# Optimization experiments

Hardware: AMD Instinct MI355X
Metric: run time of the kernel (lower is better)

## Reference

```python
import jax, jax.numpy as jnp
import numpy as np

N_EMBD = 256  # scale uses input channel dim C, per original code


def setup_inputs() -> dict:
    key = jax.random.key(0)
    k1, k2, k3, k4 = jax.random.split(key, 4)
    B, T, C, H = 512, 256, 256, 64
    x = jax.random.normal(k1, (B, T, C), dtype=jnp.float32)
    Wq = jax.random.normal(k2, (C, H), dtype=jnp.float32) * (C ** -0.5)
    Wk = jax.random.normal(k3, (C, H), dtype=jnp.float32) * (C ** -0.5)
    Wv = jax.random.normal(k4, (C, H), dtype=jnp.float32) * (C ** -0.5)
    return {"x": x, "Wq": Wq, "Wk": Wk, "Wv": Wv}


def reference(x, Wq, Wk, Wv):
    B, T, C = x.shape
    q = jnp.einsum("btc,ch->bth", x, Wq)  # [B,T,H]
    k = jnp.einsum("btc,ch->bth", x, Wk)
    v = jnp.einsum("btc,ch->bth", x, Wv)
    # Note: original scales by C**-0.5 (input dim), not head_size**-0.5.
    scores = jnp.einsum("bqh,bkh->bqk", q, k) * (C ** -0.5)  # [B,T,T]
    causal = jnp.tril(jnp.ones((T, T), dtype=bool))
    scores = jnp.where(causal, scores, -jnp.inf)
    weights = jax.nn.softmax(scores, axis=-1)
    # Dropout is identity at inference (Keras default training=False).
    out = jnp.einsum("bqk,bkh->bqh", weights, v)  # [B,T,H]
    return out
```

## Files before the change

kernel.cpp:

```cpp
#include <hip/hip_runtime.h>

#define B_  512
#define T_  256
#define C_  256
#define H_  64
#define BT_ (B_ * T_)

typedef unsigned short u16;
typedef __attribute__((ext_vector_type(8))) __bf16 bf16x8;
typedef __attribute__((ext_vector_type(8))) u16 u16x8;
typedef __attribute__((ext_vector_type(4))) float f32x4;

__device__ __forceinline__ u16 f2bf(float f) {
  union { float f; unsigned u; } v; v.f = f;
  unsigned r = v.u + 0x7fffu + ((v.u >> 16) & 1u);
  return (u16)(r >> 16);
}

__device__ __forceinline__ f32x4 mfma16(bf16x8 a, bf16x8 b, f32x4 c) {
  return __builtin_amdgcn_mfma_f32_16x16x32_bf16(a, b, c, 0, 0, 0);
}

__global__ __launch_bounds__(256) void wconv_kernel(
    const float* __restrict__ Wq, const float* __restrict__ Wk,
    const float* __restrict__ Wv, u16* __restrict__ wt) {
  int idx = blockIdx.x * 256 + threadIdx.x;
  int w   = idx >> 14;
  int rem = idx & 16383;
  int h   = rem >> 8;
  int c   = rem & 255;
  const float* W = (w == 0) ? Wq : (w == 1) ? Wk : Wv;
  wt[idx] = f2bf(W[c * H_ + h]);
}

__global__ __launch_bounds__(512, 2) void fused_kernel(
    const float* __restrict__ x, const u16* __restrict__ wt,
    float* __restrict__ out) {
  __shared__ u16 sB[2][192 * 40];
  __shared__ u16 sQ[256 * 72];
  __shared__ u16 sK[256 * 72];
  __shared__ u16 sVt[64 * 264];
  __shared__ u16 sP[8 * 16 * 88];

  const int tid  = threadIdx.x;
  const int wave = tid >> 6, lane = tid & 63;
  const int lr = lane & 15, lg = lane >> 4;
  const int b = blockIdx.x;

  const float* xb = x + (size_t)b * T_ * C_;
  float* ob = out + (size_t)b * T_ * H_;

  const f32x4 fzero = {0.f, 0.f, 0.f, 0.f};

  f32x4 acc[2][12];
#pragma unroll
  for (int mt = 0; mt < 2; ++mt)
#pragma unroll
    for (int nt = 0; nt < 12; ++nt) acc[mt][nt] = fzero;

  const float* xp0 = xb + (size_t)(wave * 32 + lr) * C_ + lg * 8;
  const float* xp1 = xp0 + 16 * C_;

  float4 aA[2][2][2];
  u16x8  breg[2][2];

#define LOAD_A(buf, kk)                                     \
  {                                                         \
    aA[buf][0][0] = *(const float4*)(xp0 + (kk) * 32);      \
    aA[buf][0][1] = *(const float4*)(xp0 + (kk) * 32 + 4);  \
    aA[buf][1][0] = *(const float4*)(xp1 + (kk) * 32);      \
    aA[buf][1][1] = *(const float4*)(xp1 + (kk) * 32 + 4);  \
  }

#define LOAD_B(buf, kk)                                                         \
  {                                                                             \
    int d0 = tid;                                                               \
    breg[buf][0] = *(const u16x8*)(wt + (d0 >> 2) * C_ + (kk) * 32 + (d0 & 3) * 8); \
    if (tid < 256) {                                                            \
      int d1 = 512 + tid;                                                       \
      breg[buf][1] = *(const u16x8*)(wt + (d1 >> 2) * C_ + (kk) * 32 + (d1 & 3) * 8); \
    }                                                                           \
  }

#define WRITE_B(buf)                                                \
  {                                                                 \
    int d0 = tid;                                                   \
    *(u16x8*)&sB[buf][(d0 >> 2) * 40 + (d0 & 3) * 8] = breg[buf][0];\
    if (tid < 256) {                                                \
      int d1 = 512 + tid;                                           \
      *(u16x8*)&sB[buf][(d1 >> 2) * 40 + (d1 & 3) * 8] = breg[buf][1];\
    }                                                               \
  }

#define COMPUTE(buf)                                                       \
  {                                                                        \
    bf16x8 af[2];                                                          \
    _Pragma("unroll") for (int mt = 0; mt < 2; ++mt) {                     \
      u16x8 au;                                                            \
      au[0] = f2bf(aA[buf][mt][0].x); au[1] = f2bf(aA[buf][mt][0].y);      \
      au[2] = f2bf(aA[buf][mt][0].z); au[3] = f2bf(aA[buf][mt][0].w);      \
      au[4] = f2bf(aA[buf][mt][1].x); au[5] = f2bf(aA[buf][mt][1].y);      \
      au[6] = f2bf(aA[buf][mt][1].z); au[7] = f2bf(aA[buf][mt][1].w);      \
      af[mt] = __builtin_bit_cast(bf16x8, au);                             \
    }                                                                      \
    _Pragma("unroll") for (int nt = 0; nt < 12; ++nt) {                    \
      bf16x8 bf = *(const bf16x8*)&sB[buf][(nt * 16 + lr) * 40 + lg * 8];  \
      acc[0][nt] = mfma16(af[0], bf, acc[0][nt]);                          \
      acc[1][nt] = mfma16(af[1], bf, acc[1][nt]);                          \
    }                                                                      \
  }

  LOAD_A(0, 0);
  LOAD_B(0, 0);
  WRITE_B(0);
  __syncthreads();

#pragma unroll
  for (int t = 0; t < 8; ++t) {
    const int cur = t & 1, nxt = cur ^ 1;
    if (t < 7) {
      LOAD_A(nxt, t + 1);
      LOAD_B(nxt, t + 1);
    }
    COMPUTE(cur);
    if (t < 7) WRITE_B(nxt);
    __syncthreads();
  }

  {
    const int rb0 = wave * 32 + lg * 4;
#pragma unroll
    for (int nt = 0; nt < 12; ++nt) {
      const int wsel = nt >> 2;
      const int h = (nt & 3) * 16 + lr;
#pragma unroll
      for (int mt = 0; mt < 2; ++mt) {
#pragma unroll
        for (int i = 0; i < 4; ++i) {
          const int r = rb0 + mt * 16 + i;
          u16 val = f2bf(acc[mt][nt][i]);
          if (wsel == 0)      sQ[r * 72 + h] = val;
          else if (wsel == 1) sK[r * 72 + h] = val;
          else                sVt[h * 264 + r] = val;
        }
      }
    }
  }
  __syncthreads();

  u16* sPw = sP + wave * 16 * 88;

#pragma unroll
  for (int ch = 0; ch < 2; ++ch) {
    const int c  = ch ? (15 - wave) : wave;
    const int r0 = c * 16;
    const int tl = c >> 2;

    bf16x8 qf[2];
#pragma unroll
    for (int ks = 0; ks < 2; ++ks)
      qf[ks] = *(const bf16x8*)&sQ[(r0 + lr) * 72 + ks * 32 + lg * 8];

    f32x4 o[4];
#pragma unroll
    for (int ht = 0; ht < 4; ++ht) o[ht] = fzero;
    float mrow[4], lrow[4];
#pragma unroll
    for (int i = 0; i < 4; ++i) { mrow[i] = -1e30f; lrow[i] = 0.f; }

    for (int t = 0; t <= tl; ++t) {
      f32x4 s[4];
#pragma unroll
      for (int nt = 0; nt < 4; ++nt) s[nt] = fzero;
#pragma unroll
      for (int ks = 0; ks < 2; ++ks) {
#pragma unroll
        for (int nt = 0; nt < 4; ++nt) {
          bf16x8 kf = *(const bf16x8*)&sK[(t * 64 + nt * 16 + lr) * 72 + ks * 32 + lg * 8];
          s[nt] = mfma16(qf[ks], kf, s[nt]);
        }
      }

      const bool diag = (t == tl);
#pragma unroll
      for (int i = 0; i < 4; ++i) {
        const int r = r0 + lg * 4 + i;
        float pv[4];
        float mx = -1e30f;
#pragma unroll
        for (int nt = 0; nt < 4; ++nt) {
          float v = s[nt][i] * 0.0625f;
          if (diag && (t * 64 + nt * 16 + lr > r)) v = -1e30f;
          pv[nt] = v;
          mx = fmaxf(mx, v);
        }
        mx = fmaxf(mx, __shfl_xor(mx, 1));
        mx = fmaxf(mx, __shfl_xor(mx, 2));
        mx = fmaxf(mx, __shfl_xor(mx, 4));
        mx = fmaxf(mx, __shfl_xor(mx, 8));
        float mnew = fmaxf(mrow[i], mx);
        float alpha = __expf(mrow[i] - mnew);
        mrow[i] = mnew;
        float rs = 0.f;
#pragma unroll
        for (int nt = 0; nt < 4; ++nt) {
          float p = __expf(pv[nt] - mnew);
          rs += p;
          sPw[(lg * 4 + i) * 88 + nt * 16 + lr] = f2bf(p);
        }
        rs += __shfl_xor(rs, 1);
        rs += __shfl_xor(rs, 2);
        rs += __shfl_xor(rs, 4);
        rs += __shfl_xor(rs, 8);
        lrow[i] = lrow[i] * alpha + rs;
#pragma unroll
        for (int ht = 0; ht < 4; ++ht) o[ht][i] *= alpha;
      }

      __builtin_amdgcn_wave_barrier();

#pragma unroll
      for (int ks2 = 0; ks2 < 2; ++ks2) {
        bf16x8 pf = *(const bf16x8*)&sPw[lr * 88 + ks2 * 32 + lg * 8];
#pragma unroll
        for (int ht = 0; ht < 4; ++ht) {
          bf16x8 vf = *(const bf16x8*)&sVt[(ht * 16 + lr) * 264 + t * 64 + ks2 * 32 + lg * 8];
          o[ht] = mfma16(pf, vf, o[ht]);
        }
      }
      __builtin_amdgcn_wave_barrier();
    }

#pragma unroll
    for (int i = 0; i < 4; ++i) {
      const float inv = 1.f / lrow[i];
      const int r = r0 + lg * 4 + i;
#pragma unroll
      for (int ht = 0; ht < 4; ++ht)
        ob[r * H_ + ht * 16 + lr] = o[ht][i] * inv;
    }
  }
#undef LOAD_A
#undef LOAD_B
#undef WRITE_B
#undef COMPUTE
}

extern "C" void kernel_launch(void* const* d_in, const int* in_sizes, int n_in,
                              void* d_out, int out_size, void* d_ws, size_t ws_size,
                              hipStream_t stream) {
  const float* x  = (const float*)d_in[0];
  const float* Wq = (const float*)d_in[1];
  const float* Wk = (const float*)d_in[2];
  const float* Wv = (const float*)d_in[3];
  float* out = (float*)d_out;

  u16* wt = (u16*)d_ws;

  wconv_kernel<<<192, 256, 0, stream>>>(Wq, Wk, Wv, wt);
  fused_kernel<<<B_, 512, 0, stream>>>(x, wt, out);
}
```

Measured before the change: 227.4 us.

## Double block to 1024 threads, one 16-row chunk per wave, alias P onto Q

The fused kernel now launches 16 waves per block instead of 8. Each wave projects 16 rows of Q/K/V rather than 32 and runs causal attention on a single 16-row query chunk, instead of a balanced pair of chunks. The separate P scratch buffer is removed: each wave writes its probabilities into its own Q rows, which it has already loaded into registers. The goal is more resident waves per CU to hide latency, at the cost of uneven attention work across waves, since later chunks need up to four key tiles while early ones need one.

```diff
diff --git a/kernel.cpp b/kernel.cpp
--- a/kernel.cpp
+++ b/kernel.cpp
@@ -33,14 +33,13 @@
   wt[idx] = f2bf(W[c * H_ + h]);
 }
 
-__global__ __launch_bounds__(512, 2) void fused_kernel(
+__global__ __launch_bounds__(1024, 4) void fused_kernel(
     const float* __restrict__ x, const u16* __restrict__ wt,
     float* __restrict__ out) {
   __shared__ u16 sB[2][192 * 40];
-  __shared__ u16 sQ[256 * 72];
+  __shared__ u16 sQP[256 * 72];
   __shared__ u16 sK[256 * 72];
   __shared__ u16 sVt[64 * 264];
-  __shared__ u16 sP[8 * 16 * 88];
 
   const int tid  = threadIdx.x;
   const int wave = tid >> 6, lane = tid & 63;
@@ -52,61 +51,48 @@
 
   const f32x4 fzero = {0.f, 0.f, 0.f, 0.f};
 
-  f32x4 acc[2][12];
-#pragma unroll
-  for (int mt = 0; mt < 2; ++mt)
-#pragma unroll
-    for (int nt = 0; nt < 12; ++nt) acc[mt][nt] = fzero;
-
-  const float* xp0 = xb + (size_t)(wave * 32 + lr) * C_ + lg * 8;
-  const float* xp1 = xp0 + 16 * C_;
-
-  float4 aA[2][2][2];
-  u16x8  breg[2][2];
+  f32x4 acc[12];
+#pragma unroll
+  for (int nt = 0; nt < 12; ++nt) acc[nt] = fzero;
+
+  const float* xp0 = xb + (size_t)(wave * 16 + lr) * C_ + lg * 8;
+
+  float4 aA[2][2];
+  u16x8  breg[2];
 
 #define LOAD_A(buf, kk)                                     \
   {                                                         \
-    aA[buf][0][0] = *(const float4*)(xp0 + (kk) * 32);      \
-    aA[buf][0][1] = *(const float4*)(xp0 + (kk) * 32 + 4);  \
-    aA[buf][1][0] = *(const float4*)(xp1 + (kk) * 32);      \
-    aA[buf][1][1] = *(const float4*)(xp1 + (kk) * 32 + 4);  \
-  }
-
-#define LOAD_B(buf, kk)                                                         \
-  {                                                                             \
-    int d0 = tid;                                                               \
-    breg[buf][0] = *(const u16x8*)(wt + (d0 >> 2) * C_ + (kk) * 32 + (d0 & 3) * 8); \
-    if (tid < 256) {                                                            \
-      int d1 = 512 + tid;                                                       \
-      breg[buf][1] = *(const u16x8*)(wt + (d1 >> 2) * C_ + (kk) * 32 + (d1 & 3) * 8); \
-    }                                                                           \
+    aA[buf][0] = *(const float4*)(xp0 + (kk) * 32);         \
+    aA[buf][1] = *(const float4*)(xp0 + (kk) * 32 + 4);     \
+  }
+
+#define LOAD_B(buf, kk)                                                        \
+  {                                                                            \
+    if (tid < 768) {                                                           \
+      int d = tid;                                                             \
+      breg[buf] = *(const u16x8*)(wt + (d >> 2) * C_ + (kk) * 32 + (d & 3) * 8); \
+    }                                                                          \
   }
 
 #define WRITE_B(buf)                                                \
   {                                                                 \
-    int d0 = tid;                                                   \
-    *(u16x8*)&sB[buf][(d0 >> 2) * 40 + (d0 & 3) * 8] = breg[buf][0];\
-    if (tid < 256) {                                                \
-      int d1 = 512 + tid;                                           \
-      *(u16x8*)&sB[buf][(d1 >> 2) * 40 + (d1 & 3) * 8] = breg[buf][1];\
+    if (tid < 768) {                                                \
+      int d = tid;                                                  \
+      *(u16x8*)&sB[buf][(d >> 2) * 40 + (d & 3) * 8] = breg[buf];   \
     }                                                               \
   }
 
 #define COMPUTE(buf)                                                       \
   {                                                                        \
-    bf16x8 af[2];                                                          \
-    _Pragma("unroll") for (int mt = 0; mt < 2; ++mt) {                     \
-      u16x8 au;                                                            \
-      au[0] = f2bf(aA[buf][mt][0].x); au[1] = f2bf(aA[buf][mt][0].y);      \
-      au[2] = f2bf(aA[buf][mt][0].z); au[3] = f2bf(aA[buf][mt][0].w);      \
-      au[4] = f2bf(aA[buf][mt][1].x); au[5] = f2bf(aA[buf][mt][1].y);      \
-      au[6] = f2bf(aA[buf][mt][1].z); au[7] = f2bf(aA[buf][mt][1].w);      \
-      af[mt] = __builtin_bit_cast(bf16x8, au);                             \
-    }                                                                      \
+    u16x8 au;                                                              \
+    au[0] = f2bf(aA[buf][0].x); au[1] = f2bf(aA[buf][0].y);                \
+    au[2] = f2bf(aA[buf][0].z); au[3] = f2bf(aA[buf][0].w);                \
+    au[4] = f2bf(aA[buf][1].x); au[5] = f2bf(aA[buf][1].y);                \
+    au[6] = f2bf(aA[buf][1].z); au[7] = f2bf(aA[buf][1].w);                \
+    bf16x8 af = __builtin_bit_cast(bf16x8, au);                            \
     _Pragma("unroll") for (int nt = 0; nt < 12; ++nt) {                    \
       bf16x8 bf = *(const bf16x8*)&sB[buf][(nt * 16 + lr) * 40 + lg * 8];  \
-      acc[0][nt] = mfma16(af[0], bf, acc[0][nt]);                          \
-      acc[1][nt] = mfma16(af[1], bf, acc[1][nt]);                          \
+      acc[nt] = mfma16(af, bf, acc[nt]);                                   \
     }                                                                      \
   }
 
@@ -128,117 +114,112 @@
   }
 
   {
-    const int rb0 = wave * 32 + lg * 4;
+    const int rb0 = wave * 16 + lg * 4;
 #pragma unroll
     for (int nt = 0; nt < 12; ++nt) {
       const int wsel = nt >> 2;
       const int h = (nt & 3) * 16 + lr;
 #pragma unroll
-      for (int mt = 0; mt < 2; ++mt) {
-#pragma unroll
-        for (int i = 0; i < 4; ++i) {
-          const int r = rb0 + mt * 16 + i;
-          u16 val = f2bf(acc[mt][nt][i]);
-          if (wsel == 0)      sQ[r * 72 + h] = val;
-          else if (wsel == 1) sK[r * 72 + h] = val;
-          else                sVt[h * 264 + r] = val;
-        }
+      for (int i = 0; i < 4; ++i) {
+        const int r = rb0 + i;
+        u16 val = f2bf(acc[nt][i]);
+        if (wsel == 0)      sQP[r * 72 + h] = val;
+        else if (wsel == 1) sK[r * 72 + h] = val;
+        else                sVt[h * 264 + r] = val;
       }
     }
   }
   __syncthreads();
 
-  u16* sPw = sP + wave * 16 * 88;
-
-#pragma unroll
-  for (int ch = 0; ch < 2; ++ch) {
-    const int c  = ch ? (15 - wave) : wave;
-    const int r0 = c * 16;
-    const int tl = c >> 2;
-
-    bf16x8 qf[2];
-#pragma unroll
-    for (int ks = 0; ks < 2; ++ks)
-      qf[ks] = *(const bf16x8*)&sQ[(r0 + lr) * 72 + ks * 32 + lg * 8];
-
-    f32x4 o[4];
-#pragma unroll
-    for (int ht = 0; ht < 4; ++ht) o[ht] = fzero;
-    float mrow[4], lrow[4];
-#pragma unroll
-    for (int i = 0; i < 4; ++i) { mrow[i] = -1e30f; lrow[i] = 0.f; }
-
-    for (int t = 0; t <= tl; ++t) {
-      f32x4 s[4];
-#pragma unroll
-      for (int nt = 0; nt < 4; ++nt) s[nt] = fzero;
-#pragma unroll
-      for (int ks = 0; ks < 2; ++ks) {
-#pragma unroll
-        for (int nt = 0; nt < 4; ++nt) {
-          bf16x8 kf = *(const bf16x8*)&sK[(t * 64 + nt * 16 + lr) * 72 + ks * 32 + lg * 8];
-          s[nt] = mfma16(qf[ks], kf, s[nt]);
-        }
-      }
-
-      const bool diag = (t == tl);
-#pragma unroll
-      for (int i = 0; i < 4; ++i) {
-        const int r = r0 + lg * 4 + i;
-        float pv[4];
-        float mx = -1e30f;
-#pragma unroll
-        for (int nt = 0; nt < 4; ++nt) {
-          float v = s[nt][i] * 0.0625f;
-          if (diag && (t * 64 + nt * 16 + lr > r)) v = -1e30f;
-          pv[nt] = v;
-          mx = fmaxf(mx, v);
-        }
-        mx = fmaxf(mx, __shfl_xor(mx, 1));
-        mx = fmaxf(mx, __shfl_xor(mx, 2));
-        mx = fmaxf(mx, __shfl_xor(mx, 4));
-        mx = fmaxf(mx, __shfl_xor(mx, 8));
-        float mnew = fmaxf(mrow[i], mx);
-        float alpha = __expf(mrow[i] - mnew);
-        mrow[i] = mnew;
-        float rs = 0.f;
-#pragma unroll
-        for (int nt = 0; nt < 4; ++nt) {
-          float p = __expf(pv[nt] - mnew);
-          rs += p;
-          sPw[(lg * 4 + i) * 88 + nt * 16 + lr] = f2bf(p);
-        }
-        rs += __shfl_xor(rs, 1);
-        rs += __shfl_xor(rs, 2);
-        rs += __shfl_xor(rs, 4);
-        rs += __shfl_xor(rs, 8);
-        lrow[i] = lrow[i] * alpha + rs;
-#pragma unroll
-        for (int ht = 0; ht < 4; ++ht) o[ht][i] *= alpha;
-      }
-
-      __builtin_amdgcn_wave_barrier();
-
-#pragma unroll
-      for (int ks2 = 0; ks2 < 2; ++ks2) {
-        bf16x8 pf = *(const bf16x8*)&sPw[lr * 88 + ks2 * 32 + lg * 8];
-#pragma unroll
-        for (int ht = 0; ht < 4; ++ht) {
-          bf16x8 vf = *(const bf16x8*)&sVt[(ht * 16 + lr) * 264 + t * 64 + ks2 * 32 + lg * 8];
-          o[ht] = mfma16(pf, vf, o[ht]);
-        }
-      }
-      __builtin_amdgcn_wave_barrier();
-    }
-
+  const int c  = wave;
+  const int r0 = c * 16;
+  const int tl = c >> 2;
+
+  bf16x8 qf[2];
+#pragma unroll
+  for (int ks = 0; ks < 2; ++ks)
+    qf[ks] = *(const bf16x8*)&sQP[(r0 + lr) * 72 + ks * 32 + lg * 8];
+  __builtin_amdgcn_wave_barrier();
+
+  u16* sPw = sQP + wave * (16 * 72);
+
+  f32x4 o[4];
+#pragma unroll
+  for (int ht = 0; ht < 4; ++ht) o[ht] = fzero;
+  float mrow[4], lrow[4];
+#pragma unroll
+  for (int i = 0; i < 4; ++i) { mrow[i] = -1e30f; lrow[i] = 0.f; }
+
+  for (int t = 0; t <= tl; ++t) {
+    f32x4 s[4];
+#pragma unroll
+    for (int nt = 0; nt < 4; ++nt) s[nt] = fzero;
+#pragma unroll
+    for (int ks = 0; ks < 2; ++ks) {
+#pragma unroll
+      for (int nt = 0; nt < 4; ++nt) {
+        bf16x8 kf = *(const bf16x8*)&sK[(t * 64 + nt * 16 + lr) * 72 + ks * 32 + lg * 8];
+        s[nt] = mfma16(qf[ks], kf, s[nt]);
+      }
+    }
+
+    const bool diag = (t == tl);
 #pragma unroll
     for (int i = 0; i < 4; ++i) {
-      const float inv = 1.f / lrow[i];
       const int r = r0 + lg * 4 + i;
-#pragma unroll
-      for (int ht = 0; ht < 4; ++ht)
-        ob[r * H_ + ht * 16 + lr] = o[ht][i] * inv;
-    }
+      float pv[4];
+      float mx = -1e30f;
+#pragma unroll
+      for (int nt = 0; nt < 4; ++nt) {
+        float v = s[nt][i] * 0.0625f;
+        if (diag && (t * 64 + nt * 16 + lr > r)) v = -1e30f;
+        pv[nt] = v;
+        mx = fmaxf(mx, v);
+      }
+      mx = fmaxf(mx, __shfl_xor(mx, 1));
+      mx = fmaxf(mx, __shfl_xor(mx, 2));
+      mx = fmaxf(mx, __shfl_xor(mx, 4));
+      mx = fmaxf(mx, __shfl_xor(mx, 8));
+      float mnew = fmaxf(mrow[i], mx);
+      float alpha = __expf(mrow[i] - mnew);
+      mrow[i] = mnew;
+      float rs = 0.f;
+#pragma unroll
+      for (int nt = 0; nt < 4; ++nt) {
+        float p = __expf(pv[nt] - mnew);
+        rs += p;
+        sPw[(lg * 4 + i) * 72 + nt * 16 + lr] = f2bf(p);
+      }
+      rs += __shfl_xor(rs, 1);
+      rs += __shfl_xor(rs, 2);
+      rs += __shfl_xor(rs, 4);
+      rs += __shfl_xor(rs, 8);
+      lrow[i] = lrow[i] * alpha + rs;
+#pragma unroll
+      for (int ht = 0; ht < 4; ++ht) o[ht][i] *= alpha;
+    }
+
+    __builtin_amdgcn_wave_barrier();
+
+#pragma unroll
+    for (int ks2 = 0; ks2 < 2; ++ks2) {
+      bf16x8 pf = *(const bf16x8*)&sPw[lr * 72 + ks2 * 32 + lg * 8];
+#pragma unroll
+      for (int ht = 0; ht < 4; ++ht) {
+        bf16x8 vf = *(const bf16x8*)&sVt[(ht * 16 + lr) * 264 + t * 64 + ks2 * 32 + lg * 8];
+        o[ht] = mfma16(pf, vf, o[ht]);
+      }
+    }
+    __builtin_amdgcn_wave_barrier();
+  }
+
+#pragma unroll
+  for (int i = 0; i < 4; ++i) {
+    const float inv = 1.f / lrow[i];
+    const int r = r0 + lg * 4 + i;
+#pragma unroll
+    for (int ht = 0; ht < 4; ++ht)
+      ob[r * H_ + ht * 16 + lr] = o[ht][i] * inv;
   }
 #undef LOAD_A
 #undef LOAD_B
@@ -258,5 +239,5 @@
   u16* wt = (u16*)d_ws;
 
   wconv_kernel<<<192, 256, 0, stream>>>(Wq, Wk, Wv, wt);
-  fused_kernel<<<B_, 512, 0, stream>>>(x, wt, out);
-}
+  fused_kernel<<<B_, 1024, 0, stream>>>(x, wt, out);
+}
```

Result: no change. 225.2 us (-1.0%).
